# Performance work log

Measured on AMD Instinct MI355X. Metric: run time of the kernel, lower is better.

Reference implementation:

```python
import jax, jax.numpy as jnp
import numpy as np

MASK_VAL = -1e18


def _soft_nn(src, src_mask, tgt, tgt_mask):
    """score[b,i,j] = -mean_d (src[b,i,d]-tgt[b,j,d])^2, masked softmax over j,
    then soft nearest neighbor = weights @ tgt.  Uses the |a|^2+|b|^2-2ab
    expansion instead of materializing the [B,M,N,D] broadcast tensor."""
    D = src.shape[-1]
    sq_s = jnp.sum(src * src, axis=-1)                 # [B,M]
    sq_t = jnp.sum(tgt * tgt, axis=-1)                 # [B,N]
    dots = jnp.einsum('bid,bjd->bij', src, tgt)        # [B,M,N]
    dist = (sq_s[:, :, None] + sq_t[:, None, :] - 2.0 * dots) / D
    valid = (src_mask[:, :, None] > 0) & (tgt_mask[:, None, :] > 0)
    score = jnp.where(valid, -dist, MASK_VAL)
    weights = jax.nn.softmax(score, axis=-1)           # [B,M,N]
    nn = jnp.einsum('bij,bjd->bid', weights, tgt)      # [B,M,D]
    return nn, weights


def _cycle_loss(mask, lens, beta):
    """Expected index under beta vs. original index; only the diagonal of the
    original [B,M,M] distance matrix survives, so compute it directly."""
    M = mask.shape[-1]
    idx = jnp.arange(M, dtype=beta.dtype)              # [M]
    index_nn = jnp.einsum('j,bij->bi', idx, beta)      # [B,M]
    l_seq = jnp.square(index_nn - idx[None, :]) * (mask > 0)  # diag of masked dist
    return jnp.mean(jnp.sum(l_seq, axis=-1) / lens)


def setup_inputs() -> dict:
    key = jax.random.key(0)
    kce, kse, kcl, ksl = jax.random.split(key, 4)
    B, M, N, D = 32, 1024, 1024, 128
    clip_lens = jax.random.randint(kcl, (B,), M // 2, M + 1)
    sent_lens = jax.random.randint(ksl, (B,), N // 2, N + 1)
    # original code requires max(lens) == padded length (idx_orig broadcast)
    clip_lens = clip_lens.at[0].set(M)
    sent_lens = sent_lens.at[0].set(N)
    clip_mask = (jnp.arange(M)[None, :] < clip_lens[:, None]).astype(jnp.float32)
    sent_mask = (jnp.arange(N)[None, :] < sent_lens[:, None]).astype(jnp.float32)
    return {
        'clip_emb': jax.random.normal(kce, (B, M, D), dtype=jnp.float32),
        'clip_mask': clip_mask,
        'clip_lens': clip_lens.astype(jnp.float32),
        'sent_emb': jax.random.normal(kse, (B, N, D), dtype=jnp.float32),
        'sent_mask': sent_mask,
        'sent_lens': sent_lens.astype(jnp.float32),
    }


def reference(clip_emb, clip_mask, clip_lens, sent_emb, sent_mask, sent_lens):
    # clip -> sent -> clip cycle
    clip_sent_nn, _ = _soft_nn(clip_emb, clip_mask, sent_emb, sent_mask)
    _, clip_beta = _soft_nn(clip_sent_nn, clip_mask, clip_emb, clip_mask)
    clip_clip_loss = _cycle_loss(clip_mask, clip_lens, clip_beta)
    # sent -> clip -> sent cycle
    sent_clip_nn, _ = _soft_nn(sent_emb, sent_mask, clip_emb, clip_mask)
    _, sent_beta = _soft_nn(sent_clip_nn, sent_mask, sent_emb, sent_mask)
    sent_sent_loss = _cycle_loss(sent_mask, sent_lens, sent_beta)
    return (clip_clip_loss, sent_sent_loss)
```

## Files before the change

kernel.cpp:

```cpp
#include <hip/hip_runtime.h>
#include <hip/hip_bf16.h>
#include <math.h>

typedef __attribute__((ext_vector_type(16))) float f32x16;
typedef __attribute__((ext_vector_type(8))) short short8;
typedef __attribute__((ext_vector_type(4))) short short4v;
typedef __attribute__((ext_vector_type(4))) unsigned uint4v;

#define BATCH 32
#define SEQ 1024
#define DIM 128
#define NBLK 512
#define TILE_BYTES 16384
#define CDOT 0.02254211097f
#define SQE_SCALE 0.011271055485f

__device__ __forceinline__ float exp2f_fast(float x) {
  float r;
  asm("v_exp_f32 %0, %1" : "=v"(r) : "v"(x));
  return r;
}

__device__ __forceinline__ unsigned cvt_pk_bf16(float lo, float hi) {
  unsigned r;
  asm("v_cvt_pk_bf16_f32 %0, %1, %2" : "=v"(r) : "v"(lo), "v"(hi));
  return r;
}

__device__ __forceinline__ unsigned vs_off(int j, int k) {
  return ((unsigned)(k >> 4) << 11) + ((unsigned)j << 5)
       + ((((unsigned)(k & 15)) << 1) ^ ((((unsigned)j >> 2) & 1) << 4));
}

__device__ __forceinline__ short4v ds_tr16(unsigned addr) {
  short4v r;
  asm volatile("ds_read_b64_tr_b16 %0, %1" : "=v"(r) : "v"(addr));
  return r;
}

typedef __attribute__((address_space(1))) const unsigned int gu32;
typedef __attribute__((address_space(3))) unsigned int lu32;
__device__ __forceinline__ void gload_lds16(const void* g, void* l) {
  __builtin_amdgcn_global_load_lds((gu32*)g, (lu32*)l, 16, 0, 0);
}

__global__ __launch_bounds__(256)
void prepack_kernel(const float* __restrict__ clip, const float* __restrict__ sent,
                    char* __restrict__ outN, float* __restrict__ sqe_all) {
  const int bid = blockIdx.x;
  const int tid = threadIdx.x;
  const float* inp = (bid < NBLK) ? clip : sent;
  const size_t row0 = (size_t)(bid & (NBLK - 1)) * 64;
  char* ot = outN + (size_t)bid * TILE_BYTES;
  #pragma unroll
  for (int it = 0; it < 8; ++it) {
    int idx = it * 256 + tid;
    int j = idx >> 5, q = idx & 31;
    float4 v = *reinterpret_cast<const float4*>(inp + (row0 + j) * DIM + q * 4);
    uint2 pk;
    pk.x = cvt_pk_bf16(v.x, v.y);
    pk.y = cvt_pk_bf16(v.z, v.w);
    *reinterpret_cast<uint2*>(ot + vs_off(j, q * 4)) = pk;
    float s = v.x * v.x + v.y * v.y + v.z * v.z + v.w * v.w;
    #pragma unroll
    for (int off = 1; off < 32; off <<= 1) s += __shfl_xor(s, off);
    if ((tid & 31) == 0) sqe_all[bid * 64 + j] = s * SQE_SCALE;
  }
}

__global__ __launch_bounds__(128, 2)
void cycle_kernel(const char* __restrict__ embN, const float* __restrict__ sqe_all,
                  const float* __restrict__ clip_lens, const float* __restrict__ sent_lens,
                  float* __restrict__ partials)
{
  __shared__ __align__(16) char VS[2][TILE_BYTES];

  const int tid = threadIdx.x;
  const int x = blockIdx.x;
  const int b   = (x & 7) + 8 * (x >> 8);
  const int mm  = (x >> 3) & 31;
  const int cyc = mm >> 4;
  const int qb  = mm & 15;

  const char* srcN = embN + (cyc ? (size_t)NBLK * TILE_BYTES : 0);
  const char* othN = embN + (cyc ? 0 : (size_t)NBLK * TILE_BYTES);
  const float* sqe_src = sqe_all + (cyc ? BATCH * SEQ : 0) + b * SEQ;
  const float* sqe_oth = sqe_all + (cyc ? 0 : BATCH * SEQ) + b * SEQ;
  const float* lens_src = cyc ? sent_lens : clip_lens;
  const float* lens_oth = cyc ? clip_lens : sent_lens;

  const int w = tid >> 6, l = tid & 63;
  const int il = l & 31, hi = l >> 5, g1 = (l >> 4) & 1;

  const char* src_tiles = srcN + (size_t)(b * 16) * TILE_BYTES;
  const char* oth_tiles = othN + (size_t)(b * 16) * TILE_BYTES;

  const int nv1 = (int)(lens_oth[b] + 0.5f);
  const int nv2 = (int)(lens_src[b] + 0.5f);
  const int nt1 = (nv1 + 63) >> 6;
  const int nt2 = (nv2 + 63) >> 6;

  auto STAGE = [&](int buf, const char* gt) {
    #pragma unroll
    for (int i = 0; i < 8; ++i)
      gload_lds16(gt + i * 2048 + tid * 16, &VS[buf][i * 2048 + tid * 16]);
  };

  STAGE(0, oth_tiles);

  const unsigned qk0 = (unsigned)(il * 32 + ((hi * 16) ^ (((il >> 2) & 1) << 4)));
  const int t16 = (l & 8) ? -16 : 16;

  short8 aq[8];
  {
    const char* qt = src_tiles + (size_t)qb * TILE_BYTES;
    const unsigned qoff = (unsigned)((w * 32 + il) * 32
                          + ((hi * 16) ^ (((il >> 2) & 1) << 4)));
    #pragma unroll
    for (int kc = 0; kc < 8; ++kc)
      aq[kc] = *reinterpret_cast<const short8*>(qt + qoff + kc * 2048);
  }

  f32x16 nn[4];
  #pragma unroll
  for (int d = 0; d < 4; ++d)
    #pragma unroll
    for (int r = 0; r < 16; ++r) nn[d][r] = 0.f;
  float lsum = 0.f;

  asm volatile("s_waitcnt vmcnt(0)" ::: "memory");
  __syncthreads();

  int cur = 0;
  for (int t = 0; t < nt1; ++t) {
    const int jb = t * 64;
    if (t + 1 < nt1) STAGE(cur ^ 1, oth_tiles + (size_t)(t + 1) * TILE_BYTES);
    else             STAGE(cur ^ 1, src_tiles);

    const char* vsc = &VS[cur][0];
    const unsigned vsb = (unsigned)(size_t)vsc;
    const unsigned trb0 = vsb + (unsigned)(g1 * 1920);
    const unsigned trb1 = trb0 + (unsigned)(128 + t16);
    const bool partial = (jb + 64) > nv1;

    #pragma unroll
    for (int jA = 0; jA < 2; ++jA) {
      f32x16 sa;
      #pragma unroll
      for (int r = 0; r < 16; ++r) sa[r] = 0.f;
      #pragma unroll
      for (int kc = 0; kc < 8; ++kc) {
        short8 ka = *reinterpret_cast<const short8*>(vsc + qk0 + jA * 1024 + kc * 2048);
        sa = __builtin_amdgcn_mfma_f32_32x32x16_bf16(ka, aq[kc], sa, 0, 0, 0);
      }
      float sqs[16];
      #pragma unroll
      for (int q = 0; q < 4; ++q) {
        float4 v = *reinterpret_cast<const float4*>(sqe_oth + jb + jA * 32 + q * 8 + hi * 4);
        sqs[q * 4 + 0] = v.x; sqs[q * 4 + 1] = v.y;
        sqs[q * 4 + 2] = v.z; sqs[q * 4 + 3] = v.w;
      }
      float p[16];
      #pragma unroll
      for (int r = 0; r < 16; ++r)
        p[r] = exp2f_fast(fmaf(sa[r], CDOT, -sqs[r]));
      if (partial) {
        #pragma unroll
        for (int r = 0; r < 16; ++r) {
          int j = jb + jA * 32 + (r & 3) + 8 * (r >> 2) + 4 * hi;
          p[r] = (j < nv1) ? p[r] : 0.f;
        }
      }
      float ls = 0.f;
      #pragma unroll
      for (int r = 0; r < 16; ++r) ls += p[r];
      lsum += ls;

      #pragma unroll
      for (int gm = 0; gm < 2; ++gm) {
        const int kap = jA * 2 + gm;
        unsigned u00 = cvt_pk_bf16(p[gm * 8 + 0], p[gm * 8 + 1]);
        unsigned u01 = cvt_pk_bf16(p[gm * 8 + 2], p[gm * 8 + 3]);
        unsigned u10 = cvt_pk_bf16(p[gm * 8 + 4], p[gm * 8 + 5]);
        unsigned u11 = cvt_pk_bf16(p[gm * 8 + 6], p[gm * 8 + 7]);
        asm volatile("v_permlane32_swap_b32 %0, %1" : "+v"(u00), "+v"(u10));
        asm volatile("v_permlane32_swap_b32 %0, %1" : "+v"(u01), "+v"(u11));
        uint4v pw; pw.x = u00; pw.y = u01; pw.z = u10; pw.w = u11;
        short8 paf = __builtin_bit_cast(short8, pw);

        short4v t0[4], t1[4];
        #pragma unroll
        for (int dblk = 0; dblk < 4; ++dblk) {
          t0[dblk] = ds_tr16(trb0 + (unsigned)(dblk * 4096 + kap * 512));
          t1[dblk] = ds_tr16(trb1 + (unsigned)(dblk * 4096 + kap * 512));
        }
        asm volatile("s_waitcnt lgkmcnt(0)" ::: "memory");
        __builtin_amdgcn_sched_barrier(0);
        #pragma unroll
        for (int dblk = 0; dblk < 4; ++dblk) {
          short8 vf = __builtin_shufflevector(t0[dblk], t1[dblk], 0, 1, 2, 3, 4, 5, 6, 7);
          nn[dblk] = __builtin_amdgcn_mfma_f32_32x32x16_bf16(vf, paf, nn[dblk], 0, 0, 0);
        }
      }
    }

    asm volatile("s_waitcnt vmcnt(0)" ::: "memory");
    __syncthreads();
    cur ^= 1;
  }

  lsum += __shfl_xor(lsum, 32);
  const float inv1 = 1.f / lsum;
  short8 aq2[8];
  #pragma unroll
  for (int kc = 0; kc < 8; ++kc) {
    const int dblk = kc >> 1, gm = kc & 1;
    unsigned u00 = cvt_pk_bf16(nn[dblk][gm * 8 + 0] * inv1, nn[dblk][gm * 8 + 1] * inv1);
    unsigned u01 = cvt_pk_bf16(nn[dblk][gm * 8 + 2] * inv1, nn[dblk][gm * 8 + 3] * inv1);
    unsigned u10 = cvt_pk_bf16(nn[dblk][gm * 8 + 4] * inv1, nn[dblk][gm * 8 + 5] * inv1);
    unsigned u11 = cvt_pk_bf16(nn[dblk][gm * 8 + 6] * inv1, nn[dblk][gm * 8 + 7] * inv1);
    asm volatile("v_permlane32_swap_b32 %0, %1" : "+v"(u00), "+v"(u10));
    asm volatile("v_permlane32_swap_b32 %0, %1" : "+v"(u01), "+v"(u11));
    uint4v pw; pw.x = u00; pw.y = u01; pw.z = u10; pw.w = u11;
    aq2[kc] = __builtin_bit_cast(short8, pw);
  }

  float l2s = 0.f, ixs = 0.f;
  for (int t = 0; t < nt2; ++t) {
    const int jb = t * 64;
    if (t + 1 < nt2) STAGE(cur ^ 1, src_tiles + (size_t)(t + 1) * TILE_BYTES);

    const char* vsc = &VS[cur][0];
    const bool partial = (jb + 64) > nv2;

    #pragma unroll
    for (int jA = 0; jA < 2; ++jA) {
      f32x16 sa;
      #pragma unroll
      for (int r = 0; r < 16; ++r) sa[r] = 0.f;
      #pragma unroll
      for (int kc = 0; kc < 8; ++kc) {
        short8 ka = *reinterpret_cast<const short8*>(vsc + qk0 + jA * 1024 + kc * 2048);
        sa = __builtin_amdgcn_mfma_f32_32x32x16_bf16(ka, aq2[kc], sa, 0, 0, 0);
      }
      float sqs[16];
      #pragma unroll
      for (int q = 0; q < 4; ++q) {
        float4 v = *reinterpret_cast<const float4*>(sqe_src + jb + jA * 32 + q * 8 + hi * 4);
        sqs[q * 4 + 0] = v.x; sqs[q * 4 + 1] = v.y;
        sqs[q * 4 + 2] = v.z; sqs[q * 4 + 3] = v.w;
      }
      float p[16];
      #pragma unroll
      for (int r = 0; r < 16; ++r)
        p[r] = exp2f_fast(fmaf(sa[r], CDOT, -sqs[r]));
      if (partial) {
        #pragma unroll
        for (int r = 0; r < 16; ++r) {
          int j = jb + jA * 32 + (r & 3) + 8 * (r >> 2) + 4 * hi;
          p[r] = (j < nv2) ? p[r] : 0.f;
        }
      }
      #pragma unroll
      for (int r = 0; r < 16; ++r) {
        l2s += p[r];
        float jc = (float)(jb + jA * 32 + (r & 3) + 8 * (r >> 2) + 4 * hi);
        ixs = fmaf(p[r], jc, ixs);
      }
    }

    asm volatile("s_waitcnt vmcnt(0)" ::: "memory");
    __syncthreads();
    cur ^= 1;
  }

  l2s += __shfl_xor(l2s, 32);
  ixs += __shfl_xor(ixs, 32);
  const int iabs = qb * 64 + w * 32 + il;
  float diff = ixs / l2s - (float)iabs;
  float s = (iabs < nv2) ? diff * diff : 0.f;
  #pragma unroll
  for (int off = 1; off < 32; off <<= 1) s += __shfl_xor(s, off);
  if (l == 0)
    partials[cyc * 1024 + (b * 16 + qb) * 2 + w] = s / ((float)nv2 * (float)BATCH);
}

__global__ void reduce_kernel(const float* __restrict__ partials, float* __restrict__ out) {
  __shared__ float red[256];
  const int c = blockIdx.x;
  float s = 0.f;
  for (int i = threadIdx.x; i < 1024; i += 256) s += partials[c * 1024 + i];
  red[threadIdx.x] = s;
  __syncthreads();
  for (int off = 128; off > 0; off >>= 1) {
    if (threadIdx.x < off) red[threadIdx.x] += red[threadIdx.x + off];
    __syncthreads();
  }
  if (threadIdx.x == 0) out[c] = red[0];
}

extern "C" void kernel_launch(void* const* d_in, const int* in_sizes, int n_in,
                              void* d_out, int out_size, void* d_ws, size_t ws_size,
                              hipStream_t stream) {
  const float* clip_emb  = (const float*)d_in[0];
  const float* clip_lens = (const float*)d_in[2];
  const float* sent_emb  = (const float*)d_in[3];
  const float* sent_lens = (const float*)d_in[5];
  float* out = (float*)d_out;
  char* wsb = (char*)d_ws;

  char*  embN    = wsb;
  float* sqe_all = (float*)(wsb + 2 * (size_t)NBLK * TILE_BYTES);
  float* parts   = sqe_all + 2 * BATCH * SEQ;

  prepack_kernel<<<2 * NBLK, 256, 0, stream>>>(clip_emb, sent_emb, embN, sqe_all);
  cycle_kernel<<<2 * NBLK, 128, 0, stream>>>(embN, sqe_all, clip_lens, sent_lens, parts);
  reduce_kernel<<<2, 256, 0, stream>>>(parts, out);
}
```

Baseline: 69.08 us.

## Quadruple query rows per block to reuse staged key tiles across more waves

Each block now covers 256 query rows with 4 waves, and each wave holds two 32-row query sub-tiles, so every LDS-staged key/value tile feeds twice as many MFMAs. The grid shrinks from 1024 to 256 blocks, which cuts redundant global-to-LDS staging per batch. The squared-norm vectors are also cached in LDS instead of being read from global memory in the inner loop. In exchange, register pressure roughly doubles (two sets of accumulators and query fragments), and the smaller grid may fill the 256 CUs less evenly.

```diff
diff --git a/kernel.cpp b/kernel.cpp
--- a/kernel.cpp
+++ b/kernel.cpp
@@ -68,19 +68,20 @@
   }
 }
 
-__global__ __launch_bounds__(128, 2)
+__global__ __launch_bounds__(256)
 void cycle_kernel(const char* __restrict__ embN, const float* __restrict__ sqe_all,
                   const float* __restrict__ clip_lens, const float* __restrict__ sent_lens,
                   float* __restrict__ partials)
 {
   __shared__ __align__(16) char VS[2][TILE_BYTES];
+  __shared__ __align__(16) float SQL[2][SEQ];
 
   const int tid = threadIdx.x;
   const int x = blockIdx.x;
-  const int b   = (x & 7) + 8 * (x >> 8);
-  const int mm  = (x >> 3) & 31;
-  const int cyc = mm >> 4;
-  const int qb  = mm & 15;
+  const int b   = (x & 7) + 8 * (x >> 6);
+  const int mm  = (x >> 3) & 7;
+  const int cyc = mm >> 2;
+  const int qb  = mm & 3;
 
   const char* srcN = embN + (cyc ? (size_t)NBLK * TILE_BYTES : 0);
   const char* othN = embN + (cyc ? 0 : (size_t)NBLK * TILE_BYTES);
@@ -102,31 +103,42 @@
 
   auto STAGE = [&](int buf, const char* gt) {
     #pragma unroll
-    for (int i = 0; i < 8; ++i)
-      gload_lds16(gt + i * 2048 + tid * 16, &VS[buf][i * 2048 + tid * 16]);
+    for (int i = 0; i < 4; ++i)
+      gload_lds16(gt + i * 4096 + tid * 16, &VS[buf][i * 4096 + tid * 16]);
   };
 
   STAGE(0, oth_tiles);
+  {
+    float4 vo = reinterpret_cast<const float4*>(sqe_oth)[tid];
+    float4 vq = reinterpret_cast<const float4*>(sqe_src)[tid];
+    reinterpret_cast<float4*>(&SQL[0][0])[tid] = vo;
+    reinterpret_cast<float4*>(&SQL[1][0])[tid] = vq;
+  }
 
   const unsigned qk0 = (unsigned)(il * 32 + ((hi * 16) ^ (((il >> 2) & 1) << 4)));
   const int t16 = (l & 8) ? -16 : 16;
 
-  short8 aq[8];
+  short8 aq[2][8];
   {
-    const char* qt = src_tiles + (size_t)qb * TILE_BYTES;
-    const unsigned qoff = (unsigned)((w * 32 + il) * 32
-                          + ((hi * 16) ^ (((il >> 2) & 1) << 4)));
-    #pragma unroll
-    for (int kc = 0; kc < 8; ++kc)
-      aq[kc] = *reinterpret_cast<const short8*>(qt + qoff + kc * 2048);
-  }
-
-  f32x16 nn[4];
-  #pragma unroll
-  for (int d = 0; d < 4; ++d)
-    #pragma unroll
-    for (int r = 0; r < 16; ++r) nn[d][r] = 0.f;
-  float lsum = 0.f;
+    const char* qt = src_tiles + (size_t)(qb * 4 + w) * TILE_BYTES;
+    #pragma unroll
+    for (int s = 0; s < 2; ++s) {
+      const unsigned qoff = (unsigned)((s * 32 + il) * 32
+                            + ((hi * 16) ^ (((il >> 2) & 1) << 4)));
+      #pragma unroll
+      for (int kc = 0; kc < 8; ++kc)
+        aq[s][kc] = *reinterpret_cast<const short8*>(qt + qoff + kc * 2048);
+    }
+  }
+
+  f32x16 nn[2][4];
+  #pragma unroll
+  for (int s = 0; s < 2; ++s)
+    #pragma unroll
+    for (int d = 0; d < 4; ++d)
+      #pragma unroll
+      for (int r = 0; r < 16; ++r) nn[s][d][r] = 0.f;
+  float lsum[2] = {0.f, 0.f};
 
   asm volatile("s_waitcnt vmcnt(0)" ::: "memory");
   __syncthreads();
@@ -145,48 +157,58 @@
 
     #pragma unroll
     for (int jA = 0; jA < 2; ++jA) {
-      f32x16 sa;
-      #pragma unroll
-      for (int r = 0; r < 16; ++r) sa[r] = 0.f;
+      f32x16 sa0, sa1;
+      #pragma unroll
+      for (int r = 0; r < 16; ++r) { sa0[r] = 0.f; sa1[r] = 0.f; }
       #pragma unroll
       for (int kc = 0; kc < 8; ++kc) {
         short8 ka = *reinterpret_cast<const short8*>(vsc + qk0 + jA * 1024 + kc * 2048);
-        sa = __builtin_amdgcn_mfma_f32_32x32x16_bf16(ka, aq[kc], sa, 0, 0, 0);
-      }
-      float sqs[16];
+        sa0 = __builtin_amdgcn_mfma_f32_32x32x16_bf16(ka, aq[0][kc], sa0, 0, 0, 0);
+        sa1 = __builtin_amdgcn_mfma_f32_32x32x16_bf16(ka, aq[1][kc], sa1, 0, 0, 0);
+      }
       #pragma unroll
       for (int q = 0; q < 4; ++q) {
-        float4 v = *reinterpret_cast<const float4*>(sqe_oth + jb + jA * 32 + q * 8 + hi * 4);
-        sqs[q * 4 + 0] = v.x; sqs[q * 4 + 1] = v.y;
-        sqs[q * 4 + 2] = v.z; sqs[q * 4 + 3] = v.w;
-      }
-      float p[16];
-      #pragma unroll
-      for (int r = 0; r < 16; ++r)
-        p[r] = exp2f_fast(fmaf(sa[r], CDOT, -sqs[r]));
+        float4 sq4 = *reinterpret_cast<const float4*>(&SQL[0][jb + jA * 32 + q * 8 + hi * 4]);
+        sa0[q*4+0] = exp2f_fast(fmaf(sa0[q*4+0], CDOT, -sq4.x));
+        sa0[q*4+1] = exp2f_fast(fmaf(sa0[q*4+1], CDOT, -sq4.y));
+        sa0[q*4+2] = exp2f_fast(fmaf(sa0[q*4+2], CDOT, -sq4.z));
+        sa0[q*4+3] = exp2f_fast(fmaf(sa0[q*4+3], CDOT, -sq4.w));
+        sa1[q*4+0] = exp2f_fast(fmaf(sa1[q*4+0], CDOT, -sq4.x));
+        sa1[q*4+1] = exp2f_fast(fmaf(sa1[q*4+1], CDOT, -sq4.y));
+        sa1[q*4+2] = exp2f_fast(fmaf(sa1[q*4+2], CDOT, -sq4.z));
+        sa1[q*4+3] = exp2f_fast(fmaf(sa1[q*4+3], CDOT, -sq4.w));
+      }
       if (partial) {
         #pragma unroll
         for (int r = 0; r < 16; ++r) {
           int j = jb + jA * 32 + (r & 3) + 8 * (r >> 2) + 4 * hi;
-          p[r] = (j < nv1) ? p[r] : 0.f;
+          if (j >= nv1) { sa0[r] = 0.f; sa1[r] = 0.f; }
         }
       }
-      float ls = 0.f;
-      #pragma unroll
-      for (int r = 0; r < 16; ++r) ls += p[r];
-      lsum += ls;
+      float ls0 = 0.f, ls1 = 0.f;
+      #pragma unroll
+      for (int r = 0; r < 16; ++r) { ls0 += sa0[r]; ls1 += sa1[r]; }
+      lsum[0] += ls0; lsum[1] += ls1;
 
       #pragma unroll
       for (int gm = 0; gm < 2; ++gm) {
         const int kap = jA * 2 + gm;
-        unsigned u00 = cvt_pk_bf16(p[gm * 8 + 0], p[gm * 8 + 1]);
-        unsigned u01 = cvt_pk_bf16(p[gm * 8 + 2], p[gm * 8 + 3]);
-        unsigned u10 = cvt_pk_bf16(p[gm * 8 + 4], p[gm * 8 + 5]);
-        unsigned u11 = cvt_pk_bf16(p[gm * 8 + 6], p[gm * 8 + 7]);
-        asm volatile("v_permlane32_swap_b32 %0, %1" : "+v"(u00), "+v"(u10));
-        asm volatile("v_permlane32_swap_b32 %0, %1" : "+v"(u01), "+v"(u11));
-        uint4v pw; pw.x = u00; pw.y = u01; pw.z = u10; pw.w = u11;
-        short8 paf = __builtin_bit_cast(short8, pw);
+        unsigned a00 = cvt_pk_bf16(sa0[gm*8+0], sa0[gm*8+1]);
+        unsigned a01 = cvt_pk_bf16(sa0[gm*8+2], sa0[gm*8+3]);
+        unsigned a10 = cvt_pk_bf16(sa0[gm*8+4], sa0[gm*8+5]);
+        unsigned a11 = cvt_pk_bf16(sa0[gm*8+6], sa0[gm*8+7]);
+        asm volatile("v_permlane32_swap_b32 %0, %1" : "+v"(a00), "+v"(a10));
+        asm volatile("v_permlane32_swap_b32 %0, %1" : "+v"(a01), "+v"(a11));
+        uint4v pw0; pw0.x = a00; pw0.y = a01; pw0.z = a10; pw0.w = a11;
+        short8 paf0 = __builtin_bit_cast(short8, pw0);
+        unsigned b00 = cvt_pk_bf16(sa1[gm*8+0], sa1[gm*8+1]);
+        unsigned b01 = cvt_pk_bf16(sa1[gm*8+2], sa1[gm*8+3]);
+        unsigned b10 = cvt_pk_bf16(sa1[gm*8+4], sa1[gm*8+5]);
+        unsigned b11 = cvt_pk_bf16(sa1[gm*8+6], sa1[gm*8+7]);
+        asm volatile("v_permlane32_swap_b32 %0, %1" : "+v"(b00), "+v"(b10));
+        asm volatile("v_permlane32_swap_b32 %0, %1" : "+v"(b01), "+v"(b11));
+        uint4v pw1; pw1.x = b00; pw1.y = b01; pw1.z = b10; pw1.w = b11;
+        short8 paf1 = __builtin_bit_cast(short8, pw1);
 
         short4v t0[4], t1[4];
         #pragma unroll
@@ -199,7 +221,8 @@
         #pragma unroll
         for (int dblk = 0; dblk < 4; ++dblk) {
           short8 vf = __builtin_shufflevector(t0[dblk], t1[dblk], 0, 1, 2, 3, 4, 5, 6, 7);
-          nn[dblk] = __builtin_amdgcn_mfma_f32_32x32x16_bf16(vf, paf, nn[dblk], 0, 0, 0);
+          nn[0][dblk] = __builtin_amdgcn_mfma_f32_32x32x16_bf16(vf, paf0, nn[0][dblk], 0, 0, 0);
+          nn[1][dblk] = __builtin_amdgcn_mfma_f32_32x32x16_bf16(vf, paf1, nn[1][dblk], 0, 0, 0);
         }
       }
     }
@@ -209,23 +232,26 @@
     cur ^= 1;
   }
 
-  lsum += __shfl_xor(lsum, 32);
-  const float inv1 = 1.f / lsum;
-  short8 aq2[8];
-  #pragma unroll
-  for (int kc = 0; kc < 8; ++kc) {
-    const int dblk = kc >> 1, gm = kc & 1;
-    unsigned u00 = cvt_pk_bf16(nn[dblk][gm * 8 + 0] * inv1, nn[dblk][gm * 8 + 1] * inv1);
-    unsigned u01 = cvt_pk_bf16(nn[dblk][gm * 8 + 2] * inv1, nn[dblk][gm * 8 + 3] * inv1);
-    unsigned u10 = cvt_pk_bf16(nn[dblk][gm * 8 + 4] * inv1, nn[dblk][gm * 8 + 5] * inv1);
-    unsigned u11 = cvt_pk_bf16(nn[dblk][gm * 8 + 6] * inv1, nn[dblk][gm * 8 + 7] * inv1);
-    asm volatile("v_permlane32_swap_b32 %0, %1" : "+v"(u00), "+v"(u10));
-    asm volatile("v_permlane32_swap_b32 %0, %1" : "+v"(u01), "+v"(u11));
-    uint4v pw; pw.x = u00; pw.y = u01; pw.z = u10; pw.w = u11;
-    aq2[kc] = __builtin_bit_cast(short8, pw);
-  }
-
-  float l2s = 0.f, ixs = 0.f;
+  short8 aq2[2][8];
+  #pragma unroll
+  for (int s = 0; s < 2; ++s) {
+    lsum[s] += __shfl_xor(lsum[s], 32);
+    const float inv1 = 1.f / lsum[s];
+    #pragma unroll
+    for (int kc = 0; kc < 8; ++kc) {
+      const int dblk = kc >> 1, gm = kc & 1;
+      unsigned u00 = cvt_pk_bf16(nn[s][dblk][gm*8+0] * inv1, nn[s][dblk][gm*8+1] * inv1);
+      unsigned u01 = cvt_pk_bf16(nn[s][dblk][gm*8+2] * inv1, nn[s][dblk][gm*8+3] * inv1);
+      unsigned u10 = cvt_pk_bf16(nn[s][dblk][gm*8+4] * inv1, nn[s][dblk][gm*8+5] * inv1);
+      unsigned u11 = cvt_pk_bf16(nn[s][dblk][gm*8+6] * inv1, nn[s][dblk][gm*8+7] * inv1);
+      asm volatile("v_permlane32_swap_b32 %0, %1" : "+v"(u00), "+v"(u10));
+      asm volatile("v_permlane32_swap_b32 %0, %1" : "+v"(u01), "+v"(u11));
+      uint4v pw; pw.x = u00; pw.y = u01; pw.z = u10; pw.w = u11;
+      aq2[s][kc] = __builtin_bit_cast(short8, pw);
+    }
+  }
+
+  float l2s[2] = {0.f, 0.f}, ixs[2] = {0.f, 0.f};
   for (int t = 0; t < nt2; ++t) {
     const int jb = t * 64;
     if (t + 1 < nt2) STAGE(cur ^ 1, src_tiles + (size_t)(t + 1) * TILE_BYTES);
@@ -235,37 +261,41 @@
 
     #pragma unroll
     for (int jA = 0; jA < 2; ++jA) {
-      f32x16 sa;
-      #pragma unroll
-      for (int r = 0; r < 16; ++r) sa[r] = 0.f;
+      f32x16 sa0, sa1;
+      #pragma unroll
+      for (int r = 0; r < 16; ++r) { sa0[r] = 0.f; sa1[r] = 0.f; }
       #pragma unroll
       for (int kc = 0; kc < 8; ++kc) {
         short8 ka = *reinterpret_cast<const short8*>(vsc + qk0 + jA * 1024 + kc * 2048);
-        sa = __builtin_amdgcn_mfma_f32_32x32x16_bf16(ka, aq2[kc], sa, 0, 0, 0);
-      }
-      float sqs[16];
+        sa0 = __builtin_amdgcn_mfma_f32_32x32x16_bf16(ka, aq2[0][kc], sa0, 0, 0, 0);
+        sa1 = __builtin_amdgcn_mfma_f32_32x32x16_bf16(ka, aq2[1][kc], sa1, 0, 0, 0);
+      }
       #pragma unroll
       for (int q = 0; q < 4; ++q) {
-        float4 v = *reinterpret_cast<const float4*>(sqe_src + jb + jA * 32 + q * 8 + hi * 4);
-        sqs[q * 4 + 0] = v.x; sqs[q * 4 + 1] = v.y;
-        sqs[q * 4 + 2] = v.z; sqs[q * 4 + 3] = v.w;
-      }
-      float p[16];
-      #pragma unroll
-      for (int r = 0; r < 16; ++r)
-        p[r] = exp2f_fast(fmaf(sa[r], CDOT, -sqs[r]));
+        float4 sq4 = *reinterpret_cast<const float4*>(&SQL[1][jb + jA * 32 + q * 8 + hi * 4]);
+        sa0[q*4+0] = exp2f_fast(fmaf(sa0[q*4+0], CDOT, -sq4.x));
+        sa0[q*4+1] = exp2f_fast(fmaf(sa0[q*4+1], CDOT, -sq4.y));
+        sa0[q*4+2] = exp2f_fast(fmaf(sa0[q*4+2], CDOT, -sq4.z));
+        sa0[q*4+3] = exp2f_fast(fmaf(sa0[q*4+3], CDOT, -sq4.w));
+        sa1[q*4+0] = exp2f_fast(fmaf(sa1[q*4+0], CDOT, -sq4.x));
+        sa1[q*4+1] = exp2f_fast(fmaf(sa1[q*4+1], CDOT, -sq4.y));
+        sa1[q*4+2] = exp2f_fast(fmaf(sa1[q*4+2], CDOT, -sq4.z));
+        sa1[q*4+3] = exp2f_fast(fmaf(sa1[q*4+3], CDOT, -sq4.w));
+      }
       if (partial) {
         #pragma unroll
         for (int r = 0; r < 16; ++r) {
           int j = jb + jA * 32 + (r & 3) + 8 * (r >> 2) + 4 * hi;
-          p[r] = (j < nv2) ? p[r] : 0.f;
+          if (j >= nv2) { sa0[r] = 0.f; sa1[r] = 0.f; }
         }
       }
       #pragma unroll
       for (int r = 0; r < 16; ++r) {
-        l2s += p[r];
         float jc = (float)(jb + jA * 32 + (r & 3) + 8 * (r >> 2) + 4 * hi);
-        ixs = fmaf(p[r], jc, ixs);
+        l2s[0] += sa0[r];
+        l2s[1] += sa1[r];
+        ixs[0] = fmaf(sa0[r], jc, ixs[0]);
+        ixs[1] = fmaf(sa1[r], jc, ixs[1]);
       }
     }
 
@@ -274,22 +304,26 @@
     cur ^= 1;
   }
 
-  l2s += __shfl_xor(l2s, 32);
-  ixs += __shfl_xor(ixs, 32);
-  const int iabs = qb * 64 + w * 32 + il;
-  float diff = ixs / l2s - (float)iabs;
-  float s = (iabs < nv2) ? diff * diff : 0.f;
-  #pragma unroll
-  for (int off = 1; off < 32; off <<= 1) s += __shfl_xor(s, off);
+  float acc = 0.f;
+  #pragma unroll
+  for (int s = 0; s < 2; ++s) {
+    l2s[s] += __shfl_xor(l2s[s], 32);
+    ixs[s] += __shfl_xor(ixs[s], 32);
+    int iabs = qb * 256 + w * 64 + s * 32 + il;
+    float diff = ixs[s] / l2s[s] - (float)iabs;
+    acc += (iabs < nv2) ? diff * diff : 0.f;
+  }
+  #pragma unroll
+  for (int off = 1; off < 32; off <<= 1) acc += __shfl_xor(acc, off);
   if (l == 0)
-    partials[cyc * 1024 + (b * 16 + qb) * 2 + w] = s / ((float)nv2 * (float)BATCH);
+    partials[cyc * 512 + (b * 4 + qb) * 4 + w] = acc / ((float)nv2 * (float)BATCH);
 }
 
 __global__ void reduce_kernel(const float* __restrict__ partials, float* __restrict__ out) {
   __shared__ float red[256];
   const int c = blockIdx.x;
   float s = 0.f;
-  for (int i = threadIdx.x; i < 1024; i += 256) s += partials[c * 1024 + i];
+  for (int i = threadIdx.x; i < 512; i += 256) s += partials[c * 512 + i];
   red[threadIdx.x] = s;
   __syncthreads();
   for (int off = 128; off > 0; off >>= 1) {
@@ -314,6 +348,6 @@
   float* parts   = sqe_all + 2 * BATCH * SEQ;
 
   prepack_kernel<<<2 * NBLK, 256, 0, stream>>>(clip_emb, sent_emb, embN, sqe_all);
-  cycle_kernel<<<2 * NBLK, 128, 0, stream>>>(embN, sqe_all, clip_lens, sent_lens, parts);
+  cycle_kernel<<<256, 256, 0, stream>>>(embN, sqe_all, clip_lens, sent_lens, parts);
   reduce_kernel<<<2, 256, 0, stream>>>(parts, out);
 }
```

Measured after the change: 80.69 us. 1.17x slower.
